# Kernel optimization log

Hardware: AMD Instinct MI355X
Metric: run time of the kernel (lower is better)

## Reference

```python
import jax, jax.numpy as jnp
import numpy as np

SUBSTEPS = 2  # fixed RK4 substeps per save interval (replaces adaptive diffrax solver)


def setup_inputs() -> dict:
    key = jax.random.key(0)
    k = jax.random.split(key, 6)
    dim, hidden, neighbors, T = 512, 2048, 512, 9
    ts = jnp.linspace(0.0, 1.0, T, dtype=jnp.float32)
    y0 = jax.random.normal(k[0], (dim,), dtype=jnp.float32)
    Dy0 = jax.random.normal(k[1], (neighbors, dim), dtype=jnp.float32) * 0.01
    W1 = jax.random.normal(k[2], (dim, hidden), dtype=jnp.float32) / np.sqrt(dim).astype(np.float32)
    b1 = jax.random.normal(k[3], (hidden,), dtype=jnp.float32) * 0.01
    W2 = jax.random.normal(k[4], (hidden, dim), dtype=jnp.float32) / np.sqrt(hidden).astype(np.float32)
    b2 = jax.random.normal(k[5], (dim,), dtype=jnp.float32) * 0.01
    return {"ts": ts, "y0": y0, "Dy0": Dy0, "W1": W1, "b1": b1, "W2": W2, "b2": b2}


def reference(ts, y0, Dy0, W1, b1, W2, b2):
    tmap = jax.tree_util.tree_map

    def f(y):  # autonomous NeuralODE vector field: 2-layer tanh MLP
        return jnp.tanh(y @ W1 + b1) @ W2 + b2

    def rhs(u):
        y, Dy = u                      # y: [dim], Dy: [neighbors, dim]
        z = y + Dy                     # [neighbors, dim]

        def second_order(z_):          # per-neighbor, z_: [dim]
            def first_order(y_):
                return jax.jvp(f, (y_,), (z_ - y_,))
            (dy, dDy1), (_, dDy2) = jax.jvp(first_order, (y,), (z_ - y,))
            return dy, 1.5 * dDy1 + 0.5 * dDy2

        dy, dDy = jax.vmap(second_order, out_axes=(None, 0))(z)
        return (dy, dDy)

    def axpy(u, k, c):
        return tmap(lambda a, b: a + c * b, u, k)

    def rk4(u, dt):
        k1 = rhs(u)
        k2 = rhs(axpy(u, k1, dt * 0.5))
        k3 = rhs(axpy(u, k2, dt * 0.5))
        k4 = rhs(axpy(u, k3, dt))
        return tmap(lambda a, a1, a2, a3, a4: a + (dt / 6.0) * (a1 + 2.0 * a2 + 2.0 * a3 + a4),
                    u, k1, k2, k3, k4)

    def interval(u, tpair):
        t0, t1 = tpair
        dt = (t1 - t0) / SUBSTEPS
        def body(u_, _):
            return rk4(u_, dt), None
        u_new, _ = jax.lax.scan(body, u, None, length=SUBSTEPS)
        return u_new, u_new

    u0 = (y0, Dy0)
    _, (ys, Dys) = jax.lax.scan(interval, u0, (ts[:-1], ts[1:]))
    ys = jnp.concatenate([y0[None], ys], axis=0)        # [T, dim]
    Dys = jnp.concatenate([Dy0[None], Dys], axis=0)     # [T, neighbors, dim]
    # pack (y, Dy) trajectories into one array: [T, 1+neighbors, dim]
    return jnp.concatenate([ys[:, None, :], Dys], axis=1)
```

## Files before the change

kernel.cpp:

```cpp
#include <hip/hip_runtime.h>
#include <hip/hip_bf16.h>

typedef __attribute__((ext_vector_type(8))) short short8;
typedef float f32x4 __attribute__((ext_vector_type(4)));

#define DIM 512
#define HID 2048
#define ROWSZ (513*512)
#define DT 0.0625f

#define WAITV(n) asm volatile("s_waitcnt vmcnt(" #n ")" ::: "memory")
#define SBAR()   asm volatile("s_barrier" ::: "memory")
typedef const __attribute__((address_space(1))) void* gas1;
typedef __attribute__((address_space(3))) void* las3;
#define GLL16(g,l,aux) __builtin_amdgcn_global_load_lds((gas1)(g),(las3)(l),16,0,aux)
#define GLL4(g,l,aux)  __builtin_amdgcn_global_load_lds((gas1)(g),(las3)(l),4,0,aux)

__device__ __forceinline__ float bf2f(unsigned short s){ return __uint_as_float(((unsigned)s)<<16); }
__device__ __forceinline__ unsigned short f2bfu(float f){ __hip_bfloat16 h=__float2bfloat16(f); return *(unsigned short*)&h; }
__device__ __forceinline__ float dot8(uint4 wq, const float* a){
  const unsigned short* ws=(const unsigned short*)&wq;
  float s=0.f;
#pragma unroll
  for(int i=0;i<8;++i) s += bf2f(ws[i])*a[i];
  return s;
}
__device__ __forceinline__ float dot8bb(uint4 wq, const unsigned short* a){
  const unsigned short* ws=(const unsigned short*)&wq;
  float s=0.f;
#pragma unroll
  for(int i=0;i<8;++i) s += bf2f(ws[i])*bf2f(a[i]);
  return s;
}

__device__ __forceinline__ void xbar(int* arr, int* gen, int target, bool lead){
  asm volatile("s_waitcnt vmcnt(0) lgkmcnt(0)" ::: "memory");
  __syncthreads();
  if (threadIdx.x == 0){
    __hip_atomic_fetch_add(arr, 1, __ATOMIC_RELAXED, __HIP_MEMORY_SCOPE_AGENT);
    if (lead){
      while (__hip_atomic_load(arr, __ATOMIC_RELAXED, __HIP_MEMORY_SCOPE_AGENT) < 32*target)
        __builtin_amdgcn_s_sleep(2);
      __hip_atomic_store(gen, target, __ATOMIC_RELAXED, __HIP_MEMORY_SCOPE_AGENT);
    } else {
      while (__hip_atomic_load(gen, __ATOMIC_RELAXED, __HIP_MEMORY_SCOPE_AGENT) < target)
        __builtin_amdgcn_s_sleep(4);
    }
  }
  __syncthreads();
}

__global__ void k_transpose_bf16(const float* __restrict__ src,
                                 __hip_bfloat16* __restrict__ dst, int R, int C) {
  __shared__ float tile[32][33];
  int c0 = blockIdx.x * 32, r0 = blockIdx.y * 32;
  int tx = threadIdx.x & 31, ty = threadIdx.x >> 5;
  for (int i = 0; i < 32; i += 8)
    tile[ty + i][tx] = src[(size_t)(r0 + ty + i) * C + c0 + tx];
  __syncthreads();
  for (int i = 0; i < 32; i += 8)
    dst[(size_t)(c0 + ty + i) * R + r0 + tx] = __float2bfloat16(tile[tx][ty + i]);
}

__global__ __launch_bounds__(512, 1) void k_persist(
    const float* __restrict__ y0, const float* __restrict__ Dy0,
    const unsigned short* __restrict__ W1t, const unsigned short* __restrict__ W2t,
    const float* __restrict__ b1, const float* __restrict__ b2,
    unsigned short* __restrict__ Vbuf, unsigned short* __restrict__ tbuf,
    float* __restrict__ yts, unsigned short* __restrict__ a_ss, float* __restrict__ pbuf,
    int* __restrict__ ctrl, float* __restrict__ out) {
  __shared__ __align__(16) short W1L[64 * 512];
  __shared__ __align__(16) short W2L[32 * 1024];
  __shared__ __align__(16) short ring[3][4096];
  __shared__ float ytL[DIM];
  __shared__ __align__(16) unsigned short asL[1024];
  __shared__ float pacc[512];
  __shared__ float c1L[64], c2L[64];
  __shared__ int bcast[2];

  const int t = threadIdx.x;
  if (t == 0) {
    int x;
    asm volatile("s_getreg_b32 %0, hwreg(HW_REG_XCC_ID)" : "=s"(x));
    x &= 7;
    bcast[0] = x;
    bcast[1] = atomicAdd(&ctrl[x], 1);
  }
  __syncthreads();
  const int xcd = bcast[0];
  const int sl  = bcast[1] & 31;
  const bool lead = (sl == 0);
  int* arr = ctrl + 64 + xcd * 64;
  int* gen = arr + 32;

  const int w = t >> 6, lane = t & 63, quad = lane >> 4, l16 = lane & 15;
  const int r8 = lane >> 3;
  const int mX = xcd * 64;
  const int nA = sl * 64;
  const int ni = sl >> 1, kq = sl & 1;
  const int nB = ni * 32;
  const int kb = kq * 1024;
  float* ytx = yts + xcd * DIM;
  unsigned short* asx = a_ss + xcd * HID;
  float* rec = pbuf + (size_t)(xcd * 16 + ni) * 2112;
  int* flg = ctrl + 576 + xcd * 16 + ni;

  const int awm = (w & 1) * 32, awn = (w >> 1) * 16;
  const int bwm = (w >> 1) * 16, bwn = (w & 1) * 16;

  f32x4 DyR = {0.f,0.f,0.f,0.f}, K1 = DyR, K2 = DyR, K3 = DyR;
  float yR = 0.f, kd1 = 0.f, kd2 = 0.f, kd3 = 0.f;
  const int erow0 = mX + bwm + quad * 4;
  const int ecol  = nB + bwn + l16;

  auto issueA = [&](int buf, int c) {
    int k0 = c * 64;
    GLL16(Vbuf + (size_t)(mX + w * 8 + r8) * DIM + k0 + (((lane & 7) ^ r8) << 3),
          &ring[buf][(w * 8) * 64], 1);
  };
  auto issueB = [&](int buf, int c) {
    int k0 = kb + c * 64;
    GLL16(tbuf + (size_t)(mX + w * 8 + r8) * HID + k0 + (((lane & 7) ^ r8) << 3),
          &ring[buf][(w * 8) * 64], 1);
  };

#pragma unroll
  for (int i = 0; i < 8; ++i) {
    int r = w * 8 + i;
    int src = ((lane & ~7) | ((lane & 7) ^ (r & 7))) << 3;
    GLL16(W1t + (size_t)(nA + r) * DIM + src, &W1L[r * 512], 0);
  }
#pragma unroll
  for (int i = 0; i < 4; ++i) {
    int r = w * 4 + i;
#pragma unroll
    for (int h2 = 0; h2 < 2; ++h2) {
      int g0 = h2 * 64 + lane;
      int src = ((g0 & ~7) | ((g0 & 7) ^ (r & 7))) << 3;
      GLL16(W2t + (size_t)(nB + r) * HID + kb + src, &W2L[r * 1024 + h2 * 512], 0);
    }
  }
  if (kq == 0) {
#pragma unroll
    for (int r = 0; r < 4; ++r) {
      float v = Dy0[(size_t)(erow0 + r) * DIM + ecol];
      DyR[r] = v;
      Vbuf[(size_t)(erow0 + r) * DIM + ecol] = f2bfu(v);
      out[DIM + (size_t)(erow0 + r) * DIM + ecol] = v;
    }
    if (t < 32) {
      float v = y0[nB + t];
      yR = v;
      ytx[nB + t] = v;
      if (xcd == 0) out[nB + t] = v;
    }
  }
  WAITV(0);
  __syncthreads();
  int barid = 1;
  xbar(arr, gen, barid++, lead);

  for (int ss = 0; ss < 16; ++ss) {
    for (int st = 0; st < 4; ++st) {
      const float cn = (st == 2) ? DT : 0.5f * DT;
      const int seq = ss * 4 + st + 1;
      {
        GLL4(ytx + w * 64 + lane, &ytL[w * 64], 1);
        issueA(0, 0); issueA(1, 1);
        WAITV(2); SBAR();
        {
          int row = t & 63, seg = t >> 6;
          float hs = 0.f;
#pragma unroll
          for (int g = 0; g < 8; ++g) {
            int lg = seg * 8 + g;
            int ps = ((lg & ~7) | ((lg & 7) ^ (row & 7))) << 3;
            hs += dot8(*(const uint4*)&W1L[row * 512 + ps], &ytL[lg * 8]);
          }
          pacc[seg * 64 + row] = hs;
        }
        __syncthreads();
        if (t < 64) {
          float hsum = b1[nA + t];
#pragma unroll
          for (int q = 0; q < 8; ++q) hsum += pacc[q * 64 + t];
          float a = tanhf(hsum);
          float ap = 1.f - a * a;
          c1L[t] = ap; c2L[t] = -a * ap;
          asx[nA + t] = f2bfu(a);
        }
        f32x4 acc0 = {0.f,0.f,0.f,0.f}, acc1 = acc0;
#pragma unroll
        for (int c = 0; c < 8; ++c) {
          if (c < 7) { WAITV(1); } else { WAITV(0); }
          SBAR();
          if (c < 6) issueA((c + 2) % 3, c + 2);
          const short* tA = ring[c % 3];
#pragma unroll
          for (int kk = 0; kk < 64; kk += 32) {
            int lg = (kk >> 3) + quad;
            int pa0 = awm + l16, pa1 = awm + 16 + l16, pb = awn + l16;
            short8 a0 = *(const short8*)&tA[pa0 * 64 + ((lg ^ (pa0 & 7)) << 3)];
            short8 a1 = *(const short8*)&tA[pa1 * 64 + ((lg ^ (pa1 & 7)) << 3)];
            int gb = c * 8 + lg;
            short8 b = *(const short8*)&W1L[pb * 512 + (((gb & ~7) | ((gb & 7) ^ (pb & 7))) << 3)];
            acc0 = __builtin_amdgcn_mfma_f32_16x16x32_bf16(a0, b, acc0, 0, 0, 0);
            acc1 = __builtin_amdgcn_mfma_f32_16x16x32_bf16(a1, b, acc1, 0, 0, 0);
          }
        }
        int row0 = mX + awm + quad * 4;
        int coln = nA + awn + l16;
        float C1 = c1L[awn + l16], C2 = c2L[awn + l16];
#pragma unroll
        for (int r = 0; r < 4; ++r) {
          float g0 = acc0[r], g1 = acc1[r];
          tbuf[(size_t)(row0 + r) * HID + coln]      = f2bfu(g0 * (C1 + C2 * g0));
          tbuf[(size_t)(row0 + 16 + r) * HID + coln] = f2bfu(g1 * (C1 + C2 * g1));
        }
      }
      xbar(arr, gen, barid++, lead);
      {
        GLL4((const unsigned short*)asx + kb + w * 128 + lane * 2, &asL[w * 128], 1);
        issueB(0, 0); issueB(1, 1);
        WAITV(2); SBAR();
        {
          int row = t & 31, seg = t >> 5;
          float ds = 0.f;
#pragma unroll
          for (int g = 0; g < 8; ++g) {
            int lg = seg * 8 + g;
            int ps = ((lg & ~7) | ((lg & 7) ^ (row & 7))) << 3;
            ds += dot8bb(*(const uint4*)&W2L[row * 1024 + ps], &asL[lg * 8]);
          }
          pacc[seg * 32 + row] = ds;
        }
        __syncthreads();
        float dyown = 0.f;
        if (t < 32) {
#pragma unroll
          for (int q = 0; q < 16; ++q) dyown += pacc[q * 32 + t];
        }
        f32x4 acc = {0.f,0.f,0.f,0.f};
#pragma unroll
        for (int c = 0; c < 16; ++c) {
          if (c < 15) { WAITV(1); } else { WAITV(0); }
          SBAR();
          if (c < 14) issueB((c + 2) % 3, c + 2);
          const short* tA = ring[c % 3];
#pragma unroll
          for (int kk = 0; kk < 64; kk += 32) {
            int lg = (kk >> 3) + quad;
            int pa = bwm + l16, pb = bwn + l16;
            short8 a = *(const short8*)&tA[pa * 64 + ((lg ^ (pa & 7)) << 3)];
            int gb = c * 8 + lg;
            short8 b = *(const short8*)&W2L[pb * 1024 + (((gb & ~7) | ((gb & 7) ^ (pb & 7))) << 3)];
            acc = __builtin_amdgcn_mfma_f32_16x16x32_bf16(a, b, acc, 0, 0, 0);
          }
        }
        if (kq == 1) {
          int lrow = bwm + quad * 4, lcol = bwn + l16;
#pragma unroll
          for (int r = 0; r < 4; ++r) rec[(lrow + r) * 32 + lcol] = acc[r];
          if (t < 32) rec[2048 + t] = dyown;
          asm volatile("s_waitcnt vmcnt(0)" ::: "memory");
          __syncthreads();
          if (t == 0)
            __hip_atomic_store(flg, seq, __ATOMIC_RELAXED, __HIP_MEMORY_SCOPE_AGENT);
        } else {
          if (t == 0) {
            while (__hip_atomic_load(flg, __ATOMIC_RELAXED, __HIP_MEMORY_SCOPE_AGENT) < seq)
              __builtin_amdgcn_s_sleep(1);
          }
          __syncthreads();
          float* pLDS = (float*)&ring[0][0];
          GLL16(rec + w * 256 + lane * 4, pLDS + w * 256, 1);
          if (w == 0) GLL4(rec + 2048 + lane, pLDS + 2048, 1);
          WAITV(0);
          __syncthreads();
          int lrow = bwm + quad * 4, lcol = bwn + l16;
          f32x4 o = acc;
#pragma unroll
          for (int r = 0; r < 4; ++r) o[r] += pLDS[(lrow + r) * 32 + lcol];
          if (st == 0) K1 = o; else if (st == 1) K2 = o; else if (st == 2) K3 = o;
          if (st < 3) {
#pragma unroll
            for (int r = 0; r < 4; ++r) {
              float v = DyR[r] + cn * o[r];
              Vbuf[(size_t)(erow0 + r) * DIM + ecol] = f2bfu(v);
            }
          } else {
            const float dt6 = DT / 6.f;
#pragma unroll
            for (int r = 0; r < 4; ++r) {
              float v = DyR[r] + dt6 * (K1[r] + 2.f * K2[r] + 2.f * K3[r] + o[r]);
              DyR[r] = v;
              Vbuf[(size_t)(erow0 + r) * DIM + ecol] = f2bfu(v);
              if (ss & 1) out[(size_t)(ss / 2 + 1) * ROWSZ + DIM + (size_t)(erow0 + r) * DIM + ecol] = v;
            }
          }
          if (t < 32) {
            float k4 = dyown + pLDS[2048 + t] + b2[nB + t];
            if (st == 0) kd1 = k4; else if (st == 1) kd2 = k4; else if (st == 2) kd3 = k4;
            if (st < 3) {
              ytx[nB + t] = yR + cn * k4;
            } else {
              yR += (DT / 6.f) * (kd1 + 2.f * kd2 + 2.f * kd3 + k4);
              ytx[nB + t] = yR;
              if ((ss & 1) && xcd == 0) out[(size_t)(ss / 2 + 1) * ROWSZ + nB + t] = yR;
            }
          }
        }
      }
      xbar(arr, gen, barid++, lead);
    }
  }
}

extern "C" void kernel_launch(void* const* d_in, const int* in_sizes, int n_in,
                              void* d_out, int out_size, void* d_ws, size_t ws_size,
                              hipStream_t stream) {
  const float* y0  = (const float*)d_in[1];
  const float* Dy0 = (const float*)d_in[2];
  const float* W1  = (const float*)d_in[3];
  const float* b1  = (const float*)d_in[4];
  const float* W2  = (const float*)d_in[5];
  const float* b2  = (const float*)d_in[6];
  float* out = (float*)d_out;

  char* p = (char*)d_ws;
  auto alloc = [&](size_t bytes) {
    char* r = p;
    p += (bytes + 255) & ~(size_t)255;
    return r;
  };
  unsigned short* W1t  = (unsigned short*)alloc((size_t)HID * DIM * 2);
  unsigned short* W2t  = (unsigned short*)alloc((size_t)DIM * HID * 2);
  unsigned short* Vbuf = (unsigned short*)alloc((size_t)DIM * DIM * 2);
  unsigned short* tbuf = (unsigned short*)alloc((size_t)DIM * HID * 2);
  float* yts  = (float*)alloc(8 * DIM * 4);
  unsigned short* a_ss = (unsigned short*)alloc(8 * HID * 2);
  float* pbuf = (float*)alloc((size_t)8 * 16 * 2112 * 4);
  int* ctrl   = (int*)alloc(8192);

  hipMemsetAsync(ctrl, 0, 8192, stream);
  k_transpose_bf16<<<dim3(HID / 32, DIM / 32), 256, 0, stream>>>(W1, (__hip_bfloat16*)W1t, DIM, HID);
  k_transpose_bf16<<<dim3(DIM / 32, HID / 32), 256, 0, stream>>>(W2, (__hip_bfloat16*)W2t, HID, DIM);
  k_persist<<<256, 512, 0, stream>>>(y0, Dy0, W1t, W2t, b1, b2,
                                     Vbuf, tbuf, yts, a_ss, pbuf, ctrl, out);
}
```

Before: 861.1 us.

## Use 32x32 MFMA with split-K LDS reduction and slot-based XCD barrier

Replaces the 16x16x32 MFMA tiles in both GEMM phases with 32x32x16 MFMAs. Each wave takes a K slice, and the partial sums are reduced through LDS before the epilogue. The counter-plus-leader barrier becomes a per-block slot array that 32 threads poll directly, which removes the leader hop. The partner-block exchange now reads rec with atomic loads instead of staging it through LDS. These changes aim to cut barrier latency and MFMA issue count, at the cost of extra LDS reduction traffic and syncthreads calls.

```diff
diff --git a/kernel.cpp b/kernel.cpp
--- a/kernel.cpp
+++ b/kernel.cpp
@@ -3,6 +3,7 @@
 
 typedef __attribute__((ext_vector_type(8))) short short8;
 typedef float f32x4 __attribute__((ext_vector_type(4)));
+typedef float f32x16 __attribute__((ext_vector_type(16)));
 
 #define DIM 512
 #define HID 2048
@@ -33,19 +34,14 @@
   return s;
 }
 
-__device__ __forceinline__ void xbar(int* arr, int* gen, int target, bool lead){
+__device__ __forceinline__ void xbar(int* slots, int sl, int target){
   asm volatile("s_waitcnt vmcnt(0) lgkmcnt(0)" ::: "memory");
   __syncthreads();
-  if (threadIdx.x == 0){
-    __hip_atomic_fetch_add(arr, 1, __ATOMIC_RELAXED, __HIP_MEMORY_SCOPE_AGENT);
-    if (lead){
-      while (__hip_atomic_load(arr, __ATOMIC_RELAXED, __HIP_MEMORY_SCOPE_AGENT) < 32*target)
-        __builtin_amdgcn_s_sleep(2);
-      __hip_atomic_store(gen, target, __ATOMIC_RELAXED, __HIP_MEMORY_SCOPE_AGENT);
-    } else {
-      while (__hip_atomic_load(gen, __ATOMIC_RELAXED, __HIP_MEMORY_SCOPE_AGENT) < target)
-        __builtin_amdgcn_s_sleep(4);
-    }
+  if (threadIdx.x == 0)
+    __hip_atomic_store(&slots[sl], target, __ATOMIC_RELAXED, __HIP_MEMORY_SCOPE_AGENT);
+  if (threadIdx.x < 32){
+    while (__hip_atomic_load(&slots[threadIdx.x], __ATOMIC_RELAXED, __HIP_MEMORY_SCOPE_AGENT) < target)
+      __builtin_amdgcn_s_sleep(1);
   }
   __syncthreads();
 }
@@ -89,11 +85,10 @@
   __syncthreads();
   const int xcd = bcast[0];
   const int sl  = bcast[1] & 31;
-  const bool lead = (sl == 0);
-  int* arr = ctrl + 64 + xcd * 64;
-  int* gen = arr + 32;
+  int* slots = ctrl + 64 + xcd * 64;
 
   const int w = t >> 6, lane = t & 63, quad = lane >> 4, l16 = lane & 15;
+  const int h = lane >> 5, l32 = lane & 31;
   const int r8 = lane >> 3;
   const int mX = xcd * 64;
   const int nA = sl * 64;
@@ -105,13 +100,15 @@
   float* rec = pbuf + (size_t)(xcd * 16 + ni) * 2112;
   int* flg = ctrl + 576 + xcd * 16 + ni;
 
-  const int awm = (w & 1) * 32, awn = (w >> 1) * 16;
+  const int kh = w & 1, ntA = (w >> 1) & 1, mtA = w >> 2;
+  const int ksB = w & 3, mtB = w >> 2;
   const int bwm = (w >> 1) * 16, bwn = (w & 1) * 16;
 
   f32x4 DyR = {0.f,0.f,0.f,0.f}, K1 = DyR, K2 = DyR, K3 = DyR;
   float yR = 0.f, kd1 = 0.f, kd2 = 0.f, kd3 = 0.f;
   const int erow0 = mX + bwm + quad * 4;
   const int ecol  = nB + bwn + l16;
+  const int lrow  = bwm + quad * 4, lcol = bwn + l16;
 
   auto issueA = [&](int buf, int c) {
     int k0 = c * 64;
@@ -158,7 +155,7 @@
   WAITV(0);
   __syncthreads();
   int barid = 1;
-  xbar(arr, gen, barid++, lead);
+  xbar(slots, sl, barid++);
 
   for (int ss = 0; ss < 16; ++ss) {
     for (int st = 0; st < 4; ++st) {
@@ -189,7 +186,11 @@
           c1L[t] = ap; c2L[t] = -a * ap;
           asx[nA + t] = f2bfu(a);
         }
-        f32x4 acc0 = {0.f,0.f,0.f,0.f}, acc1 = acc0;
+        f32x16 acc;
+#pragma unroll
+        for (int i = 0; i < 16; ++i) acc[i] = 0.f;
+        const int rowA = mtA * 32 + l32;
+        const int pbW  = ntA * 32 + l32;
 #pragma unroll
         for (int c = 0; c < 8; ++c) {
           if (c < 7) { WAITV(1); } else { WAITV(0); }
@@ -197,28 +198,36 @@
           if (c < 6) issueA((c + 2) % 3, c + 2);
           const short* tA = ring[c % 3];
 #pragma unroll
-          for (int kk = 0; kk < 64; kk += 32) {
-            int lg = (kk >> 3) + quad;
-            int pa0 = awm + l16, pa1 = awm + 16 + l16, pb = awn + l16;
-            short8 a0 = *(const short8*)&tA[pa0 * 64 + ((lg ^ (pa0 & 7)) << 3)];
-            short8 a1 = *(const short8*)&tA[pa1 * 64 + ((lg ^ (pa1 & 7)) << 3)];
+          for (int s = 0; s < 2; ++s) {
+            int lg = kh * 4 + s * 2 + h;
+            short8 av = *(const short8*)&tA[rowA * 64 + ((lg ^ (rowA & 7)) << 3)];
             int gb = c * 8 + lg;
-            short8 b = *(const short8*)&W1L[pb * 512 + (((gb & ~7) | ((gb & 7) ^ (pb & 7))) << 3)];
-            acc0 = __builtin_amdgcn_mfma_f32_16x16x32_bf16(a0, b, acc0, 0, 0, 0);
-            acc1 = __builtin_amdgcn_mfma_f32_16x16x32_bf16(a1, b, acc1, 0, 0, 0);
-          }
-        }
-        int row0 = mX + awm + quad * 4;
-        int coln = nA + awn + l16;
-        float C1 = c1L[awn + l16], C2 = c2L[awn + l16];
-#pragma unroll
-        for (int r = 0; r < 4; ++r) {
-          float g0 = acc0[r], g1 = acc1[r];
-          tbuf[(size_t)(row0 + r) * HID + coln]      = f2bfu(g0 * (C1 + C2 * g0));
-          tbuf[(size_t)(row0 + 16 + r) * HID + coln] = f2bfu(g1 * (C1 + C2 * g1));
+            short8 bv = *(const short8*)&W1L[pbW * 512 + (((gb & ~7) | ((gb & 7) ^ (pbW & 7))) << 3)];
+            acc = __builtin_amdgcn_mfma_f32_32x32x16_bf16(av, bv, acc, 0, 0, 0);
+          }
+        }
+        float* red = (float*)&ring[0][0];
+        __syncthreads();
+        if (kh) {
+          float* dst = red + (mtA * 2 + ntA) * 1024;
+#pragma unroll
+          for (int r = 0; r < 16; ++r)
+            dst[((r & 3) + 8 * (r >> 2) + 4 * h) * 32 + l32] = acc[r];
+        }
+        __syncthreads();
+        if (!kh) {
+          const float* srcp = red + (mtA * 2 + ntA) * 1024;
+          const int coln = nA + ntA * 32 + l32;
+          const float C1 = c1L[ntA * 32 + l32], C2 = c2L[ntA * 32 + l32];
+#pragma unroll
+          for (int r = 0; r < 16; ++r) {
+            int row32 = (r & 3) + 8 * (r >> 2) + 4 * h;
+            float gv = acc[r] + srcp[row32 * 32 + l32];
+            tbuf[(size_t)(mX + mtA * 32 + row32) * HID + coln] = f2bfu(gv * (C1 + C2 * gv));
+          }
         }
       }
-      xbar(arr, gen, barid++, lead);
+      xbar(slots, sl, barid++);
       {
         GLL4((const unsigned short*)asx + kb + w * 128 + lane * 2, &asL[w * 128], 1);
         issueB(0, 0); issueB(1, 1);
@@ -240,47 +249,69 @@
 #pragma unroll
           for (int q = 0; q < 16; ++q) dyown += pacc[q * 32 + t];
         }
-        f32x4 acc = {0.f,0.f,0.f,0.f};
+        f32x16 acc;
+#pragma unroll
+        for (int i = 0; i < 16; ++i) acc[i] = 0.f;
+        const int rowB = mtB * 32 + l32;
 #pragma unroll
         for (int c = 0; c < 16; ++c) {
           if (c < 15) { WAITV(1); } else { WAITV(0); }
           SBAR();
           if (c < 14) issueB((c + 2) % 3, c + 2);
           const short* tA = ring[c % 3];
-#pragma unroll
-          for (int kk = 0; kk < 64; kk += 32) {
-            int lg = (kk >> 3) + quad;
-            int pa = bwm + l16, pb = bwn + l16;
-            short8 a = *(const short8*)&tA[pa * 64 + ((lg ^ (pa & 7)) << 3)];
-            int gb = c * 8 + lg;
-            short8 b = *(const short8*)&W2L[pb * 1024 + (((gb & ~7) | ((gb & 7) ^ (pb & 7))) << 3)];
-            acc = __builtin_amdgcn_mfma_f32_16x16x32_bf16(a, b, acc, 0, 0, 0);
+          int lg = ksB * 2 + h;
+          short8 av = *(const short8*)&tA[rowB * 64 + ((lg ^ (rowB & 7)) << 3)];
+          int gb = c * 8 + lg;
+          short8 bv = *(const short8*)&W2L[l32 * 1024 + (((gb & ~7) | ((gb & 7) ^ (l32 & 7))) << 3)];
+          acc = __builtin_amdgcn_mfma_f32_32x32x16_bf16(av, bv, acc, 0, 0, 0);
+        }
+        float* red = (float*)&ring[0][0];
+        __syncthreads();
+        if (ksB) {
+          float* dst = red + ((ksB - 1) * 2 + mtB) * 1024;
+#pragma unroll
+          for (int r = 0; r < 16; ++r)
+            dst[((r & 3) + 8 * (r >> 2) + 4 * h) * 32 + l32] = acc[r];
+        }
+        __syncthreads();
+        if (!ksB) {
+#pragma unroll
+          for (int k2 = 1; k2 < 4; ++k2) {
+            const float* srcp = red + ((k2 - 1) * 2 + mtB) * 1024;
+#pragma unroll
+            for (int r = 0; r < 16; ++r)
+              acc[r] += srcp[((r & 3) + 8 * (r >> 2) + 4 * h) * 32 + l32];
           }
         }
         if (kq == 1) {
-          int lrow = bwm + quad * 4, lcol = bwn + l16;
-#pragma unroll
-          for (int r = 0; r < 4; ++r) rec[(lrow + r) * 32 + lcol] = acc[r];
+          if (!ksB) {
+#pragma unroll
+            for (int r = 0; r < 16; ++r)
+              rec[(mtB * 32 + (r & 3) + 8 * (r >> 2) + 4 * h) * 32 + l32] = acc[r];
+          }
           if (t < 32) rec[2048 + t] = dyown;
-          asm volatile("s_waitcnt vmcnt(0)" ::: "memory");
+          WAITV(0);
           __syncthreads();
           if (t == 0)
             __hip_atomic_store(flg, seq, __ATOMIC_RELAXED, __HIP_MEMORY_SCOPE_AGENT);
         } else {
+          float* fin = red;
+          if (!ksB) {
+#pragma unroll
+            for (int r = 0; r < 16; ++r)
+              fin[(mtB * 32 + (r & 3) + 8 * (r >> 2) + 4 * h) * 32 + l32] = acc[r];
+          }
+          __syncthreads();
           if (t == 0) {
             while (__hip_atomic_load(flg, __ATOMIC_RELAXED, __HIP_MEMORY_SCOPE_AGENT) < seq)
               __builtin_amdgcn_s_sleep(1);
           }
           __syncthreads();
-          float* pLDS = (float*)&ring[0][0];
-          GLL16(rec + w * 256 + lane * 4, pLDS + w * 256, 1);
-          if (w == 0) GLL4(rec + 2048 + lane, pLDS + 2048, 1);
-          WAITV(0);
-          __syncthreads();
-          int lrow = bwm + quad * 4, lcol = bwn + l16;
-          f32x4 o = acc;
-#pragma unroll
-          for (int r = 0; r < 4; ++r) o[r] += pLDS[(lrow + r) * 32 + lcol];
+          f32x4 o;
+#pragma unroll
+          for (int r = 0; r < 4; ++r)
+            o[r] = fin[(lrow + r) * 32 + lcol]
+                 + __hip_atomic_load(&rec[(lrow + r) * 32 + lcol], __ATOMIC_RELAXED, __HIP_MEMORY_SCOPE_AGENT);
           if (st == 0) K1 = o; else if (st == 1) K2 = o; else if (st == 2) K3 = o;
           if (st < 3) {
 #pragma unroll
@@ -299,7 +330,9 @@
             }
           }
           if (t < 32) {
-            float k4 = dyown + pLDS[2048 + t] + b2[nB + t];
+            float k4 = dyown
+                     + __hip_atomic_load(&rec[2048 + t], __ATOMIC_RELAXED, __HIP_MEMORY_SCOPE_AGENT)
+                     + b2[nB + t];
             if (st == 0) kd1 = k4; else if (st == 1) kd2 = k4; else if (st == 2) kd3 = k4;
             if (st < 3) {
               ytx[nB + t] = yR + cn * k4;
@@ -311,7 +344,7 @@
           }
         }
       }
-      xbar(arr, gen, barid++, lead);
+      xbar(slots, sl, barid++);
     }
   }
 }
```

New measurement: 976.9 us. 13.4% more time.
